# Optimization experiments

Measured on AMD Instinct MI355X. Metric: run time of the kernel, lower is better.

Reference implementation:

```python
import jax, jax.numpy as jnp
import numpy as np

NUM_GRAPHS = 8
N_NODES = 50000
N_EDGES = 800000
F_IN = 128
HID = 256
EPS_BN = 1e-5


def _gat(x, ei, W, a_src, a_dst, b, heads, out_dim):
    # PyG GATConv: h = x @ W -> [N, heads, out]; edge (j=src -> i=dst)
    N = x.shape[0]
    h = (x @ W).reshape(N, heads, out_dim)
    alpha_src = jnp.sum(h * a_src, axis=-1)  # [N, H]
    alpha_dst = jnp.sum(h * a_dst, axis=-1)  # [N, H]
    src, dst = ei[0], ei[1]
    e = jax.nn.leaky_relu(alpha_src[src] + alpha_dst[dst], 0.2)  # [E, H]
    # segment softmax over edges grouped by destination node
    m = jax.ops.segment_max(e, dst, num_segments=N)
    m = jnp.where(jnp.isfinite(m), m, 0.0)
    ex = jnp.exp(e - m[dst])
    denom = jax.ops.segment_sum(ex, dst, num_segments=N)
    alpha = ex / (denom[dst] + 1e-16)
    msg = h[src] * alpha[:, :, None]  # [E, H, out]
    agg = jax.ops.segment_sum(msg, dst, num_segments=N)
    return agg.reshape(N, heads * out_dim) + b


def _bn(h, gamma, beta):
    # BatchNorm over nodes (training-mode batch statistics, biased variance)
    mu = h.mean(axis=0)
    var = h.var(axis=0)
    return gamma * (h - mu) / jnp.sqrt(var + EPS_BN) + beta


def setup_inputs() -> dict:
    key = jax.random.key(0)
    ks = jax.random.split(key, 16)
    s = 0.05
    inp = {
        "x": jax.random.normal(ks[0], (N_NODES, F_IN), dtype=jnp.float32),
        "edge_index": jax.random.randint(ks[1], (2, N_EDGES), 0, N_NODES, dtype=jnp.int64) if False else jax.random.randint(ks[1], (2, N_EDGES), 0, N_NODES),
        "batch_index": jnp.sort(jax.random.randint(ks[2], (N_NODES,), 0, NUM_GRAPHS)),
        # conv1: GATConv(128, 64, heads=4)
        "W1": jax.random.normal(ks[3], (F_IN, HID), dtype=jnp.float32) * s,
        "a_src1": jax.random.normal(ks[4], (4, 64), dtype=jnp.float32) * s,
        "a_dst1": jax.random.normal(ks[5], (4, 64), dtype=jnp.float32) * s,
        "b1": jnp.zeros((HID,), jnp.float32),
        "g1": jnp.ones((HID,), jnp.float32),
        "beta1": jnp.zeros((HID,), jnp.float32),
        # conv2: GATConv(256, 256, heads=1)
        "W2": jax.random.normal(ks[6], (HID, HID), dtype=jnp.float32) * s,
        "a_src2": jax.random.normal(ks[7], (1, HID), dtype=jnp.float32) * s,
        "a_dst2": jax.random.normal(ks[8], (1, HID), dtype=jnp.float32) * s,
        "b2": jnp.zeros((HID,), jnp.float32),
        "g2": jnp.ones((HID,), jnp.float32),
        "beta2": jnp.zeros((HID,), jnp.float32),
        # q_head: Linear(512,256) -> ReLU -> Linear(256,4)
        "Wq1": jax.random.normal(ks[9], (2 * HID, HID), dtype=jnp.float32) * s,
        "bq1": jnp.zeros((HID,), jnp.float32),
        "Wq2": jax.random.normal(ks[10], (HID, 4), dtype=jnp.float32) * s,
        "bq2": jnp.zeros((4,), jnp.float32),
    }
    return inp


def reference(x, edge_index, batch_index, W1, a_src1, a_dst1, b1, g1, beta1,
              W2, a_src2, a_dst2, b2, g2, beta2, Wq1, bq1, Wq2, bq2):
    N = x.shape[0]
    loops = jnp.arange(N, dtype=edge_index.dtype)
    ei = jnp.concatenate([edge_index, jnp.stack([loops, loops])], axis=1)
    h = jax.nn.relu(_bn(_gat(x, ei, W1, a_src1, a_dst1, b1, 4, 64), g1, beta1))
    h = jax.nn.relu(_bn(_gat(h, ei, W2, a_src2, a_dst2, b2, 1, HID), g2, beta2))
    sums = jax.ops.segment_sum(h, batch_index, num_segments=NUM_GRAPHS)
    cnt = jax.ops.segment_sum(jnp.ones((N, 1), h.dtype), batch_index, num_segments=NUM_GRAPHS)
    gmean = sums / jnp.maximum(cnt, 1.0)
    ctx = jnp.concatenate([h, gmean[batch_index]], axis=1)  # [N, 512]
    q = jax.nn.relu(ctx @ Wq1 + bq1) @ Wq2 + bq2  # [N, 4]
    return (q, batch_index)
```

## Files before the change

### kernel.cpp

```cpp
#include <hip/hip_runtime.h>
#include <hip/hip_bf16.h>
#include <math.h>

#define F_IN  128
#define HIDC  256
#define NG    8
#define EPS_BN 1e-5f

typedef unsigned short u16;
typedef unsigned int   u32;
typedef __attribute__((ext_vector_type(8))) short bf16x8;
typedef __attribute__((ext_vector_type(4))) float f32x4;

static __device__ __forceinline__ float b2f(u16 u) {
    return __uint_as_float((u32)u << 16);
}
static __device__ __forceinline__ u16 f2b(float f) {
    u32 u = __float_as_uint(f);
    u32 r = (u + 0x7fffu + ((u >> 16) & 1u)) >> 16;
    return (u16)r;
}
static __device__ __forceinline__ u32 pack2(float a, float b) {
    return (u32)f2b(a) | ((u32)f2b(b) << 16);
}
static __device__ __forceinline__ float lk(float v) {
    return v >= 0.f ? v : 0.2f * v;
}

__global__ void f2b2_kernel(const float* __restrict__ in, u32* __restrict__ out, int npair) {
    int i = blockIdx.x * 256 + threadIdx.x;
    if (i >= npair) return;
    float2 v = ((const float2*)in)[i];
    out[i] = pack2(v.x, v.y);
}

__global__ void wt_kernel(const float* __restrict__ W, u16* __restrict__ WT,
                          int K, int Ncol) {
    int i = blockIdx.x * 256 + threadIdx.x;
    if (i >= K * Ncol) return;
    int n = i / K, k = i % K;
    WT[i] = f2b(W[(long)k * Ncol + n]);
}

__global__ void bn_coef_kernel(const float* __restrict__ sum,
                               const float* __restrict__ sumsq,
                               const float* __restrict__ gamma,
                               const float* __restrict__ beta,
                               float* __restrict__ scale,
                               float* __restrict__ bias, int N) {
    int c = threadIdx.x;
    float invN = 1.f / (float)N;
    float mu = sum[c] * invN;
    float var = sumsq[c] * invN - mu * mu;
    float inv = rsqrtf(var + EPS_BN);
    float sc = gamma[c] * inv;
    scale[c] = sc;
    bias[c] = beta[c] - mu * sc;
}

template <int K, int MODE>
__global__ __launch_bounds__(256)
void gemm_mfma_kernel(const u16* __restrict__ A, const u16* __restrict__ WT,
                      u16* __restrict__ C, int M,
                      const float* __restrict__ scaleA, const float* __restrict__ biasA,
                      const float* __restrict__ wsrc, const float* __restrict__ wdst,
                      float* __restrict__ asrc, float* __restrict__ adst,
                      const float* __restrict__ gproj, const int* __restrict__ bat,
                      const float* __restrict__ bq1) {
    __shared__ u16 sB[128][K + 8];
    int tid = threadIdx.x;
    int n0 = blockIdx.x * 128;

    constexpr int ROWCH = K * 2 / 16;
    const uint4* src = (const uint4*)(WT + (size_t)n0 * K);
    for (int i = tid; i < 128 * ROWCH; i += 256) {
        int r = i / ROWCH, c = i % ROWCH;
        *(uint4*)&sB[r][c * 8] = src[i];
    }
    __syncthreads();

    int wid = tid >> 6, lane = tid & 63;
    int row = lane & 15, quad = lane >> 4;
    int m0 = blockIdx.y * 128 + wid * 32;
    int mf0 = m0, mf1 = m0 + 16;
    bool v0 = mf0 < M, v1 = mf1 < M;
    if (!v0) return;
    const u16* Ap0 = A + (size_t)(mf0 + row) * K + quad * 8;
    const u16* Ap1 = A + (size_t)((v1 ? mf1 : mf0) + row) * K + quad * 8;

    f32x4 acc[2][8];
#pragma unroll
    for (int f = 0; f < 2; ++f)
#pragma unroll
        for (int t = 0; t < 8; ++t) acc[f][t] = (f32x4){0.f, 0.f, 0.f, 0.f};

#pragma unroll
    for (int k0 = 0; k0 < K; k0 += 32) {
        bf16x8 a[2];
        a[0] = *(const bf16x8*)(Ap0 + k0);
        a[1] = *(const bf16x8*)(Ap1 + k0);
        if constexpr (MODE != 0) {
            int c0 = k0 + quad * 8;
            float4 s0 = *(const float4*)(scaleA + c0);
            float4 s1 = *(const float4*)(scaleA + c0 + 4);
            float4 b0 = *(const float4*)(biasA + c0);
            float4 b1 = *(const float4*)(biasA + c0 + 4);
#pragma unroll
            for (int f = 0; f < 2; ++f) {
                float xv[8];
#pragma unroll
                for (int j = 0; j < 8; ++j) xv[j] = b2f((u16)a[f][j]);
                xv[0] = fmaxf(fmaf(s0.x, xv[0], b0.x), 0.f);
                xv[1] = fmaxf(fmaf(s0.y, xv[1], b0.y), 0.f);
                xv[2] = fmaxf(fmaf(s0.z, xv[2], b0.z), 0.f);
                xv[3] = fmaxf(fmaf(s0.w, xv[3], b0.w), 0.f);
                xv[4] = fmaxf(fmaf(s1.x, xv[4], b1.x), 0.f);
                xv[5] = fmaxf(fmaf(s1.y, xv[5], b1.y), 0.f);
                xv[6] = fmaxf(fmaf(s1.z, xv[6], b1.z), 0.f);
                xv[7] = fmaxf(fmaf(s1.w, xv[7], b1.w), 0.f);
#pragma unroll
                for (int j = 0; j < 8; ++j) a[f][j] = (short)f2b(xv[j]);
            }
        }
#pragma unroll
        for (int t = 0; t < 8; ++t) {
            bf16x8 b = *(const bf16x8*)&sB[t * 16 + row][k0 + quad * 8];
            acc[0][t] = __builtin_amdgcn_mfma_f32_16x16x32_bf16(a[0], b, acc[0][t], 0, 0, 0);
            acc[1][t] = __builtin_amdgcn_mfma_f32_16x16x32_bf16(a[1], b, acc[1][t], 0, 0, 0);
        }
    }

    int mf[2] = {mf0, mf1};
    bool vf[2] = {v0, v1};
    if constexpr (MODE == 2) {
#pragma unroll
        for (int f = 0; f < 2; ++f) {
            if (!vf[f]) continue;
            int bm[4];
#pragma unroll
            for (int r = 0; r < 4; ++r) bm[r] = bat[mf[f] + quad * 4 + r];
#pragma unroll
            for (int t = 0; t < 8; ++t) {
                int n = n0 + t * 16 + row;
                float bq = bq1[n];
#pragma unroll
                for (int r = 0; r < 4; ++r) {
                    float v = acc[f][t][r] + gproj[bm[r] * HIDC + n] + bq;
                    C[(size_t)(mf[f] + quad * 4 + r) * HIDC + n] = f2b(fmaxf(v, 0.f));
                }
            }
        }
    } else {
#pragma unroll
        for (int f = 0; f < 2; ++f) {
            if (!vf[f]) continue;
#pragma unroll
            for (int t = 0; t < 8; ++t) {
                int n = n0 + t * 16 + row;
#pragma unroll
                for (int r = 0; r < 4; ++r)
                    C[(size_t)(mf[f] + quad * 4 + r) * HIDC + n] = f2b(acc[f][t][r]);
            }
        }
        if constexpr (MODE == 0) {
            float pa[2][2][4] = {}, pd[2][2][4] = {};
#pragma unroll
            for (int t = 0; t < 8; ++t) {
                float ws = wsrc[n0 + t * 16 + row];
                float wd = wdst[n0 + t * 16 + row];
                int hf = t >> 2;
#pragma unroll
                for (int f = 0; f < 2; ++f)
#pragma unroll
                    for (int r = 0; r < 4; ++r) {
                        pa[f][hf][r] = fmaf(acc[f][t][r], ws, pa[f][hf][r]);
                        pd[f][hf][r] = fmaf(acc[f][t][r], wd, pd[f][hf][r]);
                    }
            }
#pragma unroll
            for (int off = 1; off < 16; off <<= 1)
#pragma unroll
                for (int f = 0; f < 2; ++f)
#pragma unroll
                    for (int hf = 0; hf < 2; ++hf)
#pragma unroll
                        for (int r = 0; r < 4; ++r) {
                            pa[f][hf][r] += __shfl_xor(pa[f][hf][r], off, 64);
                            pd[f][hf][r] += __shfl_xor(pd[f][hf][r], off, 64);
                        }
            if (row == 0) {
                int hbase = n0 >> 6;
#pragma unroll
                for (int f = 0; f < 2; ++f) {
                    if (!vf[f]) continue;
#pragma unroll
                    for (int r = 0; r < 4; ++r) {
                        int m = mf[f] + quad * 4 + r;
#pragma unroll
                        for (int hf = 0; hf < 2; ++hf) {
                            asrc[m * 4 + hbase + hf] = pa[f][hf][r];
                            adst[m * 4 + hbase + hf] = pd[f][hf][r];
                        }
                    }
                }
            }
        }
        if constexpr (MODE == 1) {
            float pa[2][4] = {}, pd[2][4] = {};
#pragma unroll
            for (int t = 0; t < 8; ++t) {
                float ws = wsrc[n0 + t * 16 + row];
                float wd = wdst[n0 + t * 16 + row];
#pragma unroll
                for (int f = 0; f < 2; ++f)
#pragma unroll
                    for (int r = 0; r < 4; ++r) {
                        pa[f][r] = fmaf(acc[f][t][r], ws, pa[f][r]);
                        pd[f][r] = fmaf(acc[f][t][r], wd, pd[f][r]);
                    }
            }
#pragma unroll
            for (int off = 1; off < 16; off <<= 1)
#pragma unroll
                for (int f = 0; f < 2; ++f)
#pragma unroll
                    for (int r = 0; r < 4; ++r) {
                        pa[f][r] += __shfl_xor(pa[f][r], off, 64);
                        pd[f][r] += __shfl_xor(pd[f][r], off, 64);
                    }
            if (row == 0) {
#pragma unroll
                for (int f = 0; f < 2; ++f) {
                    if (!vf[f]) continue;
#pragma unroll
                    for (int r = 0; r < 4; ++r) {
                        int m = mf[f] + quad * 4 + r;
                        atomicAdd(&asrc[m], pa[f][r]);
                        atomicAdd(&adst[m], pd[f][r]);
                    }
                }
            }
        }
    }
}

__global__ void deg_kernel(const int* __restrict__ ei, int E, int N,
                           int* __restrict__ deg) {
    int e = blockIdx.x * blockDim.x + threadIdx.x;
    if (e >= E + N) return;
    int d = (e < E) ? ei[E + e] : (e - E);
    atomicAdd(&deg[d], 1);
}

__global__ __launch_bounds__(256)
void scan_phase1(const int* __restrict__ deg, int* __restrict__ part,
                 int* __restrict__ bsum, int N) {
    __shared__ int tmp[256];
    int i = blockIdx.x * 256 + threadIdx.x;
    int v = (i < N) ? deg[i] : 0;
    tmp[threadIdx.x] = v;
    __syncthreads();
    for (int off = 1; off < 256; off <<= 1) {
        int t = (threadIdx.x >= off) ? tmp[threadIdx.x - off] : 0;
        __syncthreads();
        tmp[threadIdx.x] += t;
        __syncthreads();
    }
    if (i < N) part[i] = tmp[threadIdx.x];
    if (threadIdx.x == 255) bsum[blockIdx.x] = tmp[255];
}
__global__ __launch_bounds__(256)
void scan_phase2(int* __restrict__ bsum, int nb) {
    __shared__ int tmp[256];
    int v = (threadIdx.x < nb) ? bsum[threadIdx.x] : 0;
    tmp[threadIdx.x] = v;
    __syncthreads();
    for (int off = 1; off < 256; off <<= 1) {
        int t = (threadIdx.x >= off) ? tmp[threadIdx.x - off] : 0;
        __syncthreads();
        tmp[threadIdx.x] += t;
        __syncthreads();
    }
    if (threadIdx.x < nb)
        bsum[threadIdx.x] = threadIdx.x ? tmp[threadIdx.x - 1] : 0;
}
__global__ __launch_bounds__(256)
void scan_phase3(const int* __restrict__ part, const int* __restrict__ bsum,
                 int* __restrict__ rowptr, int N) {
    int i = blockIdx.x * 256 + threadIdx.x;
    if (i < N) rowptr[i + 1] = part[i] + bsum[blockIdx.x];
    if (i == 0) rowptr[0] = 0;
}

__global__ void fill_kernel(const int* __restrict__ ei, int E, int N,
                            const int* __restrict__ rowptr,
                            int* __restrict__ cur, int* __restrict__ csr_src) {
    int e = blockIdx.x * blockDim.x + threadIdx.x;
    if (e >= E + N) return;
    int s = (e < E) ? ei[e] : (e - E);
    int d = (e < E) ? ei[E + e] : (e - E);
    int pos = rowptr[d] + atomicAdd(&cur[d], 1);
    csr_src[pos] = s;
}

template <int H>
__global__ __launch_bounds__(256)
void gat_gather_kernel(const int* __restrict__ rowptr,
                       const int* __restrict__ csr_src,
                       const float* __restrict__ asrc,
                       const float* __restrict__ adst,
                       const u16* __restrict__ h,
                       u16* __restrict__ agg, int N) {
    __shared__ __align__(16) float s_alpha[4][64 * H];
    __shared__ int s_src[4][64];
    int wid = threadIdx.x >> 6, lane = threadIdx.x & 63;
    int n = blockIdx.x * 4 + wid;
    if (n >= N) return;
    int start = rowptr[n], end = rowptr[n + 1];
    float ad[H];
#pragma unroll
    for (int hh = 0; hh < H; ++hh) ad[hh] = adst[n * H + hh];

    float m[H], d[H];
#pragma unroll
    for (int hh = 0; hh < H; ++hh) { m[hh] = -1e30f; d[hh] = 0.f; }
    for (int i = start + lane; i < end; i += 64) {
        int s = csr_src[i];
        float av[H];
        if (H == 4) {
            float4 a4 = *(const float4*)(asrc + s * 4);
            av[0] = a4.x; av[1 % H] = a4.y; av[2 % H] = a4.z; av[3 % H] = a4.w;
        } else {
            av[0] = asrc[s];
        }
#pragma unroll
        for (int hh = 0; hh < H; ++hh) {
            float v = lk(av[hh] + ad[hh]);
            float mn = fmaxf(m[hh], v);
            d[hh] = fmaf(d[hh], __expf(m[hh] - mn), __expf(v - mn));
            m[hh] = mn;
        }
    }
#pragma unroll
    for (int off = 1; off < 64; off <<= 1)
#pragma unroll
        for (int hh = 0; hh < H; ++hh) {
            float mo = __shfl_xor(m[hh], off, 64);
            float dd = __shfl_xor(d[hh], off, 64);
            float mn = fmaxf(m[hh], mo);
            d[hh] = d[hh] * __expf(m[hh] - mn) + dd * __expf(mo - mn);
            m[hh] = mn;
        }
    float invd[H];
#pragma unroll
    for (int hh = 0; hh < H; ++hh) invd[hh] = 1.f / (d[hh] + 1e-16f);

    float acc0 = 0.f, acc1 = 0.f, acc2 = 0.f, acc3 = 0.f;
    const int head = (H == 4) ? (lane >> 4) : 0;
    const uint2* hp = (const uint2*)h;
    for (int base = start; base < end; base += 64) {
        int cnt = min(64, end - base);
        if (lane < cnt) {
            int s = csr_src[base + lane];
            s_src[wid][lane] = s;
            if (H == 4) {
                float4 a4 = *(const float4*)(asrc + s * 4);
                float4 av;
                av.x = __expf(lk(a4.x + ad[0]) - m[0]) * invd[0];
                av.y = __expf(lk(a4.y + ad[1 % H]) - m[1 % H]) * invd[1 % H];
                av.z = __expf(lk(a4.z + ad[2 % H]) - m[2 % H]) * invd[2 % H];
                av.w = __expf(lk(a4.w + ad[3 % H]) - m[3 % H]) * invd[3 % H];
                *(float4*)&s_alpha[wid][lane * 4] = av;
            } else {
                s_alpha[wid][lane] = __expf(lk(asrc[s] + ad[0]) - m[0]) * invd[0];
            }
        }
#define GBODY(J) { int s_ = s_src[wid][(J)];                                   \
            float al_ = s_alpha[wid][(H == 4) ? ((J) * 4 + head) : (J)];       \
            uint2 hv_ = hp[(u32)s_ * 64u + (u32)lane];                         \
            acc0 = fmaf(__uint_as_float(hv_.x << 16), al_, acc0);              \
            acc1 = fmaf(__uint_as_float(hv_.x & 0xffff0000u), al_, acc1);      \
            acc2 = fmaf(__uint_as_float(hv_.y << 16), al_, acc2);              \
            acc3 = fmaf(__uint_as_float(hv_.y & 0xffff0000u), al_, acc3); }
        int j = 0;
        for (; j + 4 <= cnt; j += 4) { GBODY(j) GBODY(j + 1) GBODY(j + 2) GBODY(j + 3) }
        for (; j < cnt; ++j) GBODY(j)
#undef GBODY
    }
    uint2 o;
    o.x = pack2(acc0, acc1);
    o.y = pack2(acc2, acc3);
    ((uint2*)(agg + (size_t)n * HIDC))[lane] = o;
}

__global__ __launch_bounds__(256)
void bn_stats_kernel(const u16* __restrict__ h, int N,
                     float* __restrict__ sum, float* __restrict__ sumsq) {
    int c = threadIdx.x;
    int r0 = blockIdx.x * 128;
    int rend = min(r0 + 128, N);
    float s = 0.f, q = 0.f;
    for (int r = r0; r < rend; ++r) {
        float v = b2f(h[(long)r * HIDC + c]);
        s += v;
        q += v * v;
    }
    atomicAdd(&sum[c], s);
    atomicAdd(&sumsq[c], q);
}

__global__ __launch_bounds__(256)
void pool_bn_kernel(const u16* __restrict__ h, const int* __restrict__ batch,
                    int N, const float* __restrict__ scale,
                    const float* __restrict__ bias,
                    float* __restrict__ gsum, float* __restrict__ gcnt) {
    int c = threadIdx.x;
    float sc = scale[c], bi = bias[c];
    int r0 = blockIdx.x * 128;
    int rend = min(r0 + 128, N);
    int curb = -1;
    float acc = 0.f;
    for (int r = r0; r < rend; ++r) {
        int b = batch[r];
        if (b != curb) {
            if (curb >= 0) atomicAdd(&gsum[curb * HIDC + c], acc);
            curb = b; acc = 0.f;
        }
        acc += fmaxf(fmaf(sc, b2f(h[(long)r * HIDC + c]), bi), 0.f);
    }
    if (curb >= 0) atomicAdd(&gsum[curb * HIDC + c], acc);
    if (c == 0) {
        int prev = -1; float cnt = 0.f;
        for (int r = r0; r < rend; ++r) {
            int b = batch[r];
            if (b != prev) {
                if (prev >= 0) atomicAdd(&gcnt[prev], cnt);
                prev = b; cnt = 0.f;
            }
            cnt += 1.f;
        }
        if (prev >= 0) atomicAdd(&gcnt[prev], cnt);
    }
}

__global__ __launch_bounds__(256)
void gmean_gproj_kernel(const float* __restrict__ gsum,
                        const float* __restrict__ gcnt,
                        const float* __restrict__ Wq1,
                        float* __restrict__ gproj) {
    int b = blockIdx.x, c = threadIdx.x;
    __shared__ float gm[HIDC];
    gm[c] = gsum[b * HIDC + c] / fmaxf(gcnt[b], 1.f);
    __syncthreads();
    float acc = 0.f;
    for (int k = 0; k < HIDC; ++k)
        acc = fmaf(gm[k], Wq1[(long)(HIDC + k) * HIDC + c], acc);
    gproj[b * HIDC + c] = acc;
}

__global__ __launch_bounds__(256)
void q_kernel(const u16* __restrict__ hid, const float* __restrict__ Wq2,
              const float* __restrict__ bq2, const int* __restrict__ batch,
              float* __restrict__ out, int N) {
    __shared__ float w[HIDC * 4];
    int t = threadIdx.x;
#pragma unroll
    for (int j = 0; j < 4; ++j) w[t + 256 * j] = Wq2[t + 256 * j];
    __syncthreads();
    int wid = t >> 6, lane = t & 63;
    int n = blockIdx.x * 4 + wid;
    if (n >= N) return;
    float a0 = 0, a1 = 0, a2 = 0, a3 = 0;
#pragma unroll
    for (int it = 0; it < 4; ++it) {
        int k = it * 64 + lane;
        float v = b2f(hid[(long)n * HIDC + k]);
        a0 = fmaf(v, w[k * 4 + 0], a0);
        a1 = fmaf(v, w[k * 4 + 1], a1);
        a2 = fmaf(v, w[k * 4 + 2], a2);
        a3 = fmaf(v, w[k * 4 + 3], a3);
    }
    for (int o = 32; o > 0; o >>= 1) {
        a0 += __shfl_down(a0, o, 64);
        a1 += __shfl_down(a1, o, 64);
        a2 += __shfl_down(a2, o, 64);
        a3 += __shfl_down(a3, o, 64);
    }
    if (lane == 0) {
        out[(long)n * 4 + 0] = a0 + bq2[0];
        out[(long)n * 4 + 1] = a1 + bq2[1];
        out[(long)n * 4 + 2] = a2 + bq2[2];
        out[(long)n * 4 + 3] = a3 + bq2[3];
        out[(long)N * 4 + n] = (float)batch[n];
    }
}

extern "C" void kernel_launch(void* const* d_in, const int* in_sizes, int n_in,
                              void* d_out, int out_size, void* d_ws, size_t ws_size,
                              hipStream_t stream) {
    const float* x   = (const float*)d_in[0];
    const int*   ei  = (const int*)d_in[1];
    const int*   bat = (const int*)d_in[2];
    const float* W1  = (const float*)d_in[3];
    const float* as1 = (const float*)d_in[4];
    const float* ad1 = (const float*)d_in[5];
    const float* g1  = (const float*)d_in[7];
    const float* be1 = (const float*)d_in[8];
    const float* W2  = (const float*)d_in[9];
    const float* as2 = (const float*)d_in[10];
    const float* ad2 = (const float*)d_in[11];
    const float* g2  = (const float*)d_in[13];
    const float* be2 = (const float*)d_in[14];
    const float* Wq1 = (const float*)d_in[15];
    const float* bq1 = (const float*)d_in[16];
    const float* Wq2 = (const float*)d_in[17];
    const float* bq2 = (const float*)d_in[18];
    float* out = (float*)d_out;

    const int N = in_sizes[0] / F_IN;
    const int E = in_sizes[1] / 2;
    const int Etot = E + N;
    const int nb = (N + 255) / 256;

    const size_t hbytes = (size_t)N * HIDC * sizeof(u16);
    char* p = (char*)d_ws;
    auto alloc = [&](size_t sz) { char* q = p; p += (sz + 255) & ~(size_t)255; return q; };
    u16* BX   = (u16*)alloc((size_t)N * F_IN * sizeof(u16));
    u16* BH   = (u16*)alloc(hbytes);
    u16* BA   = (u16*)alloc(hbytes);
    u16* WT1  = (u16*)alloc((size_t)HIDC * F_IN * sizeof(u16));
    u16* WT2  = (u16*)alloc((size_t)HIDC * HIDC * sizeof(u16));
    u16* WQT  = (u16*)alloc((size_t)HIDC * HIDC * sizeof(u16));
    float* asrc = (float*)alloc((size_t)N * 4 * 4 * 2);
    float* adst = asrc + (size_t)N * 4;
    int* rowptr  = (int*)alloc((size_t)(N + 1) * 4);
    int* csr_src = (int*)alloc((size_t)Etot * 4);
    int* cur     = (int*)alloc((size_t)N * 4 * 2);
    int* cur2    = cur + N;
    int* part    = (int*)alloc((size_t)N * 4);
    int* bsum    = (int*)alloc((size_t)nb * 4);
    float* bnsum = (float*)alloc(HIDC * 4 * 2);
    float* bnsq  = bnsum + HIDC;
    float* sc1   = (float*)alloc(HIDC * 4);
    float* bi1   = (float*)alloc(HIDC * 4);
    float* sc2   = (float*)alloc(HIDC * 4);
    float* bi2   = (float*)alloc(HIDC * 4);
    float* gsum  = (float*)alloc((NG * HIDC + NG) * 4);
    float* gcnt  = gsum + NG * HIDC;
    float* gproj = (float*)alloc(NG * HIDC * 4);

    dim3 gemmGrid(2, (N + 127) / 128);
    int edgeBlocks = (Etot + 255) / 256;
    int nodeBlocksW = (N + 3) / 4;

    hipMemsetAsync(cur, 0, (size_t)N * 4 * 2, stream);
    deg_kernel<<<edgeBlocks, 256, 0, stream>>>(ei, E, N, cur);
    scan_phase1<<<nb, 256, 0, stream>>>(cur, part, bsum, N);
    scan_phase2<<<1, 256, 0, stream>>>(bsum, nb);
    scan_phase3<<<nb, 256, 0, stream>>>(part, bsum, rowptr, N);
    fill_kernel<<<edgeBlocks, 256, 0, stream>>>(ei, E, N, rowptr, cur2, csr_src);

    f2b2_kernel<<<(N * F_IN / 2 + 255) / 256, 256, 0, stream>>>(x, (u32*)BX, N * F_IN / 2);
    wt_kernel<<<(F_IN * HIDC + 255) / 256, 256, 0, stream>>>(W1, WT1, F_IN, HIDC);
    wt_kernel<<<(HIDC * HIDC + 255) / 256, 256, 0, stream>>>(W2, WT2, HIDC, HIDC);
    wt_kernel<<<(HIDC * HIDC + 255) / 256, 256, 0, stream>>>(Wq1, WQT, HIDC, HIDC);

    gemm_mfma_kernel<F_IN, 0><<<gemmGrid, 256, 0, stream>>>(
        BX, WT1, BH, N, nullptr, nullptr, as1, ad1, asrc, adst, nullptr, nullptr, nullptr);
    gat_gather_kernel<4><<<nodeBlocksW, 256, 0, stream>>>(rowptr, csr_src, asrc, adst, BH, BA, N);
    hipMemsetAsync(bnsum, 0, HIDC * 4 * 2, stream);
    bn_stats_kernel<<<(N + 127) / 128, 256, 0, stream>>>(BA, N, bnsum, bnsq);
    bn_coef_kernel<<<1, HIDC, 0, stream>>>(bnsum, bnsq, g1, be1, sc1, bi1, N);

    hipMemsetAsync(asrc, 0, (size_t)N * 4 * 4 * 2, stream);
    gemm_mfma_kernel<HIDC, 1><<<gemmGrid, 256, 0, stream>>>(
        BA, WT2, BH, N, sc1, bi1, as2, ad2, asrc, adst, nullptr, nullptr, nullptr);
    gat_gather_kernel<1><<<nodeBlocksW, 256, 0, stream>>>(rowptr, csr_src, asrc, adst, BH, BA, N);
    hipMemsetAsync(bnsum, 0, HIDC * 4 * 2, stream);
    bn_stats_kernel<<<(N + 127) / 128, 256, 0, stream>>>(BA, N, bnsum, bnsq);
    bn_coef_kernel<<<1, HIDC, 0, stream>>>(bnsum, bnsq, g2, be2, sc2, bi2, N);

    hipMemsetAsync(gsum, 0, (NG * HIDC + NG) * 4, stream);
    pool_bn_kernel<<<(N + 127) / 128, 256, 0, stream>>>(BA, bat, N, sc2, bi2, gsum, gcnt);
    gmean_gproj_kernel<<<NG, HIDC, 0, stream>>>(gsum, gcnt, Wq1, gproj);

    gemm_mfma_kernel<HIDC, 2><<<gemmGrid, 256, 0, stream>>>(
        BA, WQT, BH, N, sc2, bi2, nullptr, nullptr, nullptr, nullptr, gproj, bat, bq1);
    q_kernel<<<nodeBlocksW, 256, 0, stream>>>(BH, Wq2, bq2, bat, out, N);
}
```

Before: 552.5 us.

## Fuse q-head output into GEMM epilogue, merge prep kernels, precompute gather offsets

The second q-head Linear (256->4) now runs inside the MODE-2 GEMM epilogue. It uses per-lane FMAs, a shuffle reduction and atomic adds into the output, which is pre-initialized with the bias and batch index. This removes the bf16 hidden-buffer write and the separate q_kernel read. The conversion and transpose kernels are merged into one prep launch. The gather kernel stores precomputed byte offsets together with the attention weights in one shared array and uses packed FMAs. The atomics make the summation order nondeterministic and add an extra init launch.

```diff
diff --git a/kernel.cpp b/kernel.cpp
--- a/kernel.cpp
+++ b/kernel.cpp
@@ -11,6 +11,7 @@
 typedef unsigned int   u32;
 typedef __attribute__((ext_vector_type(8))) short bf16x8;
 typedef __attribute__((ext_vector_type(4))) float f32x4;
+typedef __attribute__((ext_vector_type(2))) float f32x2;
 
 static __device__ __forceinline__ float b2f(u16 u) {
     return __uint_as_float((u32)u << 16);
@@ -27,19 +28,44 @@
     return v >= 0.f ? v : 0.2f * v;
 }
 
-__global__ void f2b2_kernel(const float* __restrict__ in, u32* __restrict__ out, int npair) {
+__global__ void prep_kernel(const float* __restrict__ x,
+                            const float* __restrict__ W1,
+                            const float* __restrict__ W2,
+                            const float* __restrict__ Wq1,
+                            u32* __restrict__ xb, u16* __restrict__ WT1,
+                            u16* __restrict__ WT2, u16* __restrict__ WQT,
+                            int npair) {
     int i = blockIdx.x * 256 + threadIdx.x;
-    if (i >= npair) return;
-    float2 v = ((const float2*)in)[i];
-    out[i] = pack2(v.x, v.y);
-}
-
-__global__ void wt_kernel(const float* __restrict__ W, u16* __restrict__ WT,
-                          int K, int Ncol) {
+    if (i < npair) {
+        float2 v = ((const float2*)x)[i];
+        xb[i] = pack2(v.x, v.y);
+        return;
+    }
+    i -= npair;
+    if (i < F_IN * HIDC) {
+        int nn = i / F_IN, k = i % F_IN;
+        WT1[i] = f2b(W1[(long)k * HIDC + nn]);
+        return;
+    }
+    i -= F_IN * HIDC;
+    if (i < HIDC * HIDC) {
+        int nn = i / HIDC, k = i % HIDC;
+        WT2[i] = f2b(W2[(long)k * HIDC + nn]);
+        return;
+    }
+    i -= HIDC * HIDC;
+    if (i < HIDC * HIDC) {
+        int nn = i / HIDC, k = i % HIDC;
+        WQT[i] = f2b(Wq1[(long)k * HIDC + nn]);
+    }
+}
+
+__global__ void out_init_kernel(float* __restrict__ out,
+                                const float* __restrict__ bq2,
+                                const int* __restrict__ batch, int N) {
     int i = blockIdx.x * 256 + threadIdx.x;
-    if (i >= K * Ncol) return;
-    int n = i / K, k = i % K;
-    WT[i] = f2b(W[(long)k * Ncol + n]);
+    if (i < N * 4) out[i] = bq2[i & 3];
+    else if (i < N * 5) out[i] = (float)batch[i - N * 4];
 }
 
 __global__ void bn_coef_kernel(const float* __restrict__ sum,
@@ -66,7 +92,8 @@
                       const float* __restrict__ wsrc, const float* __restrict__ wdst,
                       float* __restrict__ asrc, float* __restrict__ adst,
                       const float* __restrict__ gproj, const int* __restrict__ bat,
-                      const float* __restrict__ bq1) {
+                      const float* __restrict__ bq1,
+                      const float* __restrict__ wq2, float* __restrict__ qout) {
     __shared__ u16 sB[128][K + 8];
     int tid = threadIdx.x;
     int n0 = blockIdx.x * 128;
@@ -133,6 +160,13 @@
     int mf[2] = {mf0, mf1};
     bool vf[2] = {v0, v1};
     if constexpr (MODE == 2) {
+        float qacc[2][4][4];
+#pragma unroll
+        for (int f = 0; f < 2; ++f)
+#pragma unroll
+            for (int r = 0; r < 4; ++r)
+#pragma unroll
+                for (int j = 0; j < 4; ++j) qacc[f][r][j] = 0.f;
 #pragma unroll
         for (int f = 0; f < 2; ++f) {
             if (!vf[f]) continue;
@@ -143,10 +177,36 @@
             for (int t = 0; t < 8; ++t) {
                 int n = n0 + t * 16 + row;
                 float bq = bq1[n];
+                float4 w4 = ((const float4*)wq2)[n];
 #pragma unroll
                 for (int r = 0; r < 4; ++r) {
-                    float v = acc[f][t][r] + gproj[bm[r] * HIDC + n] + bq;
-                    C[(size_t)(mf[f] + quad * 4 + r) * HIDC + n] = f2b(fmaxf(v, 0.f));
+                    float v = fmaxf(acc[f][t][r] + gproj[bm[r] * HIDC + n] + bq, 0.f);
+                    qacc[f][r][0] = fmaf(v, w4.x, qacc[f][r][0]);
+                    qacc[f][r][1] = fmaf(v, w4.y, qacc[f][r][1]);
+                    qacc[f][r][2] = fmaf(v, w4.z, qacc[f][r][2]);
+                    qacc[f][r][3] = fmaf(v, w4.w, qacc[f][r][3]);
+                }
+            }
+        }
+#pragma unroll
+        for (int off = 1; off < 16; off <<= 1)
+#pragma unroll
+            for (int f = 0; f < 2; ++f)
+#pragma unroll
+                for (int r = 0; r < 4; ++r)
+#pragma unroll
+                    for (int j = 0; j < 4; ++j)
+                        qacc[f][r][j] += __shfl_xor(qacc[f][r][j], off, 64);
+        if (row == 0) {
+#pragma unroll
+            for (int f = 0; f < 2; ++f) {
+                if (!vf[f]) continue;
+#pragma unroll
+                for (int r = 0; r < 4; ++r) {
+                    size_t m = mf[f] + quad * 4 + r;
+#pragma unroll
+                    for (int j = 0; j < 4; ++j)
+                        atomicAdd(&qout[m * 4 + j], qacc[f][r][j]);
                 }
             }
         }
@@ -311,8 +371,7 @@
                        const float* __restrict__ adst,
                        const u16* __restrict__ h,
                        u16* __restrict__ agg, int N) {
-    __shared__ __align__(16) float s_alpha[4][64 * H];
-    __shared__ int s_src[4][64];
+    __shared__ __align__(16) uint2 s_ed[4][64 * H];
     int wid = threadIdx.x >> 6, lane = threadIdx.x & 63;
     int n = blockIdx.x * 4 + wid;
     if (n >= N) return;
@@ -355,41 +414,52 @@
 #pragma unroll
     for (int hh = 0; hh < H; ++hh) invd[hh] = 1.f / (d[hh] + 1e-16f);
 
-    float acc0 = 0.f, acc1 = 0.f, acc2 = 0.f, acc3 = 0.f;
+    f32x2 acc01 = {0.f, 0.f}, acc23 = {0.f, 0.f};
     const int head = (H == 4) ? (lane >> 4) : 0;
-    const uint2* hp = (const uint2*)h;
+    const char* hb = (const char*)h;
+    const u32 laneB = (u32)lane * 8u;
     for (int base = start; base < end; base += 64) {
         int cnt = min(64, end - base);
         if (lane < cnt) {
             int s = csr_src[base + lane];
-            s_src[wid][lane] = s;
+            u32 off = (u32)s * (u32)(HIDC * 2);
             if (H == 4) {
                 float4 a4 = *(const float4*)(asrc + s * 4);
-                float4 av;
-                av.x = __expf(lk(a4.x + ad[0]) - m[0]) * invd[0];
-                av.y = __expf(lk(a4.y + ad[1 % H]) - m[1 % H]) * invd[1 % H];
-                av.z = __expf(lk(a4.z + ad[2 % H]) - m[2 % H]) * invd[2 % H];
-                av.w = __expf(lk(a4.w + ad[3 % H]) - m[3 % H]) * invd[3 % H];
-                *(float4*)&s_alpha[wid][lane * 4] = av;
+                uint4 w0, w1;
+                w0.x = off;
+                w0.y = __float_as_uint(__expf(lk(a4.x + ad[0]) - m[0]) * invd[0]);
+                w0.z = off;
+                w0.w = __float_as_uint(__expf(lk(a4.y + ad[1 % H]) - m[1 % H]) * invd[1 % H]);
+                w1.x = off;
+                w1.y = __float_as_uint(__expf(lk(a4.z + ad[2 % H]) - m[2 % H]) * invd[2 % H]);
+                w1.z = off;
+                w1.w = __float_as_uint(__expf(lk(a4.w + ad[3 % H]) - m[3 % H]) * invd[3 % H]);
+                *(uint4*)&s_ed[wid][lane * 4] = w0;
+                *(uint4*)&s_ed[wid][lane * 4 + 2] = w1;
             } else {
-                s_alpha[wid][lane] = __expf(lk(asrc[s] + ad[0]) - m[0]) * invd[0];
-            }
-        }
-#define GBODY(J) { int s_ = s_src[wid][(J)];                                   \
-            float al_ = s_alpha[wid][(H == 4) ? ((J) * 4 + head) : (J)];       \
-            uint2 hv_ = hp[(u32)s_ * 64u + (u32)lane];                         \
-            acc0 = fmaf(__uint_as_float(hv_.x << 16), al_, acc0);              \
-            acc1 = fmaf(__uint_as_float(hv_.x & 0xffff0000u), al_, acc1);      \
-            acc2 = fmaf(__uint_as_float(hv_.y << 16), al_, acc2);              \
-            acc3 = fmaf(__uint_as_float(hv_.y & 0xffff0000u), al_, acc3); }
+                float al = __expf(lk(asrc[s] + ad[0]) - m[0]) * invd[0];
+                s_ed[wid][lane] = make_uint2(off, __float_as_uint(al));
+            }
+        }
+#define GBODY(J) {                                                             \
+            uint2 e_ = s_ed[wid][(H == 4) ? ((J) * 4 + head) : (J)];           \
+            const uint2 hv_ = *(const uint2*)(hb + (size_t)(e_.x + laneB));    \
+            float al_ = __uint_as_float(e_.y);                                 \
+            f32x2 al2_ = {al_, al_};                                           \
+            f32x2 v01_ = { __uint_as_float(hv_.x << 16),                       \
+                           __uint_as_float(hv_.x & 0xffff0000u) };             \
+            f32x2 v23_ = { __uint_as_float(hv_.y << 16),                       \
+                           __uint_as_float(hv_.y & 0xffff0000u) };             \
+            acc01 = __builtin_elementwise_fma(v01_, al2_, acc01);              \
+            acc23 = __builtin_elementwise_fma(v23_, al2_, acc23); }
         int j = 0;
         for (; j + 4 <= cnt; j += 4) { GBODY(j) GBODY(j + 1) GBODY(j + 2) GBODY(j + 3) }
         for (; j < cnt; ++j) GBODY(j)
 #undef GBODY
     }
     uint2 o;
-    o.x = pack2(acc0, acc1);
-    o.y = pack2(acc2, acc3);
+    o.x = pack2(acc01.x, acc01.y);
+    o.y = pack2(acc23.x, acc23.y);
     ((uint2*)(agg + (size_t)n * HIDC))[lane] = o;
 }
 
@@ -456,43 +526,6 @@
     for (int k = 0; k < HIDC; ++k)
         acc = fmaf(gm[k], Wq1[(long)(HIDC + k) * HIDC + c], acc);
     gproj[b * HIDC + c] = acc;
-}
-
-__global__ __launch_bounds__(256)
-void q_kernel(const u16* __restrict__ hid, const float* __restrict__ Wq2,
-              const float* __restrict__ bq2, const int* __restrict__ batch,
-              float* __restrict__ out, int N) {
-    __shared__ float w[HIDC * 4];
-    int t = threadIdx.x;
-#pragma unroll
-    for (int j = 0; j < 4; ++j) w[t + 256 * j] = Wq2[t + 256 * j];
-    __syncthreads();
-    int wid = t >> 6, lane = t & 63;
-    int n = blockIdx.x * 4 + wid;
-    if (n >= N) return;
-    float a0 = 0, a1 = 0, a2 = 0, a3 = 0;
-#pragma unroll
-    for (int it = 0; it < 4; ++it) {
-        int k = it * 64 + lane;
-        float v = b2f(hid[(long)n * HIDC + k]);
-        a0 = fmaf(v, w[k * 4 + 0], a0);
-        a1 = fmaf(v, w[k * 4 + 1], a1);
-        a2 = fmaf(v, w[k * 4 + 2], a2);
-        a3 = fmaf(v, w[k * 4 + 3], a3);
-    }
-    for (int o = 32; o > 0; o >>= 1) {
-        a0 += __shfl_down(a0, o, 64);
-        a1 += __shfl_down(a1, o, 64);
-        a2 += __shfl_down(a2, o, 64);
-        a3 += __shfl_down(a3, o, 64);
-    }
-    if (lane == 0) {
-        out[(long)n * 4 + 0] = a0 + bq2[0];
-        out[(long)n * 4 + 1] = a1 + bq2[1];
-        out[(long)n * 4 + 2] = a2 + bq2[2];
-        out[(long)n * 4 + 3] = a3 + bq2[3];
-        out[(long)N * 4 + n] = (float)batch[n];
-    }
 }
 
 extern "C" void kernel_launch(void* const* d_in, const int* in_sizes, int n_in,
@@ -552,6 +585,8 @@
     dim3 gemmGrid(2, (N + 127) / 128);
     int edgeBlocks = (Etot + 255) / 256;
     int nodeBlocksW = (N + 3) / 4;
+    int npair = N * F_IN / 2;
+    int prepTotal = npair + F_IN * HIDC + 2 * HIDC * HIDC;
 
     hipMemsetAsync(cur, 0, (size_t)N * 4 * 2, stream);
     deg_kernel<<<edgeBlocks, 256, 0, stream>>>(ei, E, N, cur);
@@ -560,13 +595,12 @@
     scan_phase3<<<nb, 256, 0, stream>>>(part, bsum, rowptr, N);
     fill_kernel<<<edgeBlocks, 256, 0, stream>>>(ei, E, N, rowptr, cur2, csr_src);
 
-    f2b2_kernel<<<(N * F_IN / 2 + 255) / 256, 256, 0, stream>>>(x, (u32*)BX, N * F_IN / 2);
-    wt_kernel<<<(F_IN * HIDC + 255) / 256, 256, 0, stream>>>(W1, WT1, F_IN, HIDC);
-    wt_kernel<<<(HIDC * HIDC + 255) / 256, 256, 0, stream>>>(W2, WT2, HIDC, HIDC);
-    wt_kernel<<<(HIDC * HIDC + 255) / 256, 256, 0, stream>>>(Wq1, WQT, HIDC, HIDC);
+    prep_kernel<<<(prepTotal + 255) / 256, 256, 0, stream>>>(
+        x, W1, W2, Wq1, (u32*)BX, WT1, WT2, WQT, npair);
 
     gemm_mfma_kernel<F_IN, 0><<<gemmGrid, 256, 0, stream>>>(
-        BX, WT1, BH, N, nullptr, nullptr, as1, ad1, asrc, adst, nullptr, nullptr, nullptr);
+        BX, WT1, BH, N, nullptr, nullptr, as1, ad1, asrc, adst,
+        nullptr, nullptr, nullptr, nullptr, nullptr);
     gat_gather_kernel<4><<<nodeBlocksW, 256, 0, stream>>>(rowptr, csr_src, asrc, adst, BH, BA, N);
     hipMemsetAsync(bnsum, 0, HIDC * 4 * 2, stream);
     bn_stats_kernel<<<(N + 127) / 128, 256, 0, stream>>>(BA, N, bnsum, bnsq);
@@ -574,7 +608,8 @@
 
     hipMemsetAsync(asrc, 0, (size_t)N * 4 * 4 * 2, stream);
     gemm_mfma_kernel<HIDC, 1><<<gemmGrid, 256, 0, stream>>>(
-        BA, WT2, BH, N, sc1, bi1, as2, ad2, asrc, adst, nullptr, nullptr, nullptr);
+        BA, WT2, BH, N, sc1, bi1, as2, ad2, asrc, adst,
+        nullptr, nullptr, nullptr, nullptr, nullptr);
     gat_gather_kernel<1><<<nodeBlocksW, 256, 0, stream>>>(rowptr, csr_src, asrc, adst, BH, BA, N);
     hipMemsetAsync(bnsum, 0, HIDC * 4 * 2, stream);
     bn_stats_kernel<<<(N + 127) / 128, 256, 0, stream>>>(BA, N, bnsum, bnsq);
@@ -583,8 +618,9 @@
     hipMemsetAsync(gsum, 0, (NG * HIDC + NG) * 4, stream);
     pool_bn_kernel<<<(N + 127) / 128, 256, 0, stream>>>(BA, bat, N, sc2, bi2, gsum, gcnt);
     gmean_gproj_kernel<<<NG, HIDC, 0, stream>>>(gsum, gcnt, Wq1, gproj);
+    out_init_kernel<<<(N * 5 + 255) / 256, 256, 0, stream>>>(out, bq2, bat, N);
 
     gemm_mfma_kernel<HIDC, 2><<<gemmGrid, 256, 0, stream>>>(
-        BA, WQT, BH, N, sc2, bi2, nullptr, nullptr, nullptr, nullptr, gproj, bat, bq1);
-    q_kernel<<<nodeBlocksW, 256, 0, stream>>>(BH, Wq2, bq2, bat, out, N);
-}
+        BA, WQT, nullptr, N, sc2, bi2, nullptr, nullptr, nullptr, nullptr,
+        gproj, bat, bq1, Wq2, out);
+}
```

Result: slower. 564.4 us (+2.1%).
